# Kernel tuning notes

Measured on AMD Instinct MI355X. Metric: run time of the kernel, lower is better.

## Reference

```python
import jax, jax.numpy as jnp
import numpy as np


def setup_inputs() -> dict:
    key = jax.random.key(0)
    ks = jax.random.split(key, 4)
    B, C, D, H, W = 2, 128, 16, 16, 16
    scale = 1.0 / np.sqrt(C)
    x = jax.random.normal(ks[0], (B, C, D, H, W), dtype=jnp.float32)
    Wq = jax.random.normal(ks[1], (C, C), dtype=jnp.float32) * scale
    Wk = jax.random.normal(ks[2], (C, C), dtype=jnp.float32) * scale
    Wv = jax.random.normal(ks[3], (C, C), dtype=jnp.float32) * scale
    bq = jnp.zeros((C,), jnp.float32)
    bk = jnp.zeros((C,), jnp.float32)
    bv = jnp.zeros((C,), jnp.float32)
    gamma = jnp.asarray(0.3, jnp.float32)
    return {"x": x, "Wq": Wq, "bq": bq, "Wk": Wk, "bk": bk, "Wv": Wv, "bv": bv, "gamma": gamma}


def reference(x, Wq, bq, Wk, bk, Wv, bv, gamma):
    B, C, D, H, W = x.shape
    N = D * H * W
    xf = x.reshape(B, C, N)  # flatten spatial dims
    # 1x1x1 Conv3d == per-voxel channel mixing
    q = jnp.einsum('oc,bcn->bon', Wq, xf) + bq[:, None]
    k = jnp.einsum('oc,bcn->bon', Wk, xf) + bk[:, None]
    v = jnp.einsum('oc,bcn->bon', Wv, xf) + bv[:, None]
    # attn[b,n,m] = sum_c q[b,c,n] * k[b,c,m], custom 1.3 scale, softmax over m
    attn = jax.nn.softmax(jnp.einsum('bcn,bcm->bnm', q, k) * 1.3, axis=2)
    # out = v @ attn^T : out[b,c,n] = sum_m v[b,c,m] * attn[b,n,m]
    out = jnp.einsum('bcm,bnm->bcn', v, attn)
    return x + gamma * out.reshape(B, C, D, H, W)
```

## Files before the change

### kernel.cpp

```cpp
#include <hip/hip_runtime.h>
#include <hip/hip_bf16.h>

typedef __bf16 bf16x8 __attribute__((ext_vector_type(8)));
typedef __bf16 bf16x4 __attribute__((ext_vector_type(4)));
typedef float  floatx4 __attribute__((ext_vector_type(4)));


#define QSCALE 1.8755035f

__global__ __launch_bounds__(128) void proj_kernel(
    const float* __restrict__ x,
    const float* __restrict__ Wq, const float* __restrict__ bq,
    const float* __restrict__ Wk, const float* __restrict__ bk,
    const float* __restrict__ Wv, const float* __restrict__ bv,
    __bf16* __restrict__ qT, __bf16* __restrict__ kT, __bf16* __restrict__ vT2)
{
    constexpr int C = 128, N = 4096;
    const int b = blockIdx.z, which = blockIdx.y, n0 = blockIdx.x * 32;
    const int tid = threadIdx.x;
    const int wv = tid >> 6, lane = tid & 63, l15 = lane & 15, quad = lane >> 4;
    const float* W    = (which == 0) ? Wq : (which == 1) ? Wk : Wv;
    const float* bias = (which == 0) ? bq : (which == 1) ? bk : bv;

    __shared__ __bf16 xhi[32][136];
    __shared__ __bf16 xlo[32][136];
    __shared__ __bf16 v_lds[128][40];

    #pragma unroll
    for (int rep = 0; rep < 8; ++rep) {
        const int j = tid + rep * 128;
        const int c = j >> 3, nl4 = (j & 7) * 4;
        const float4 xv = *(const float4*)(x + (size_t)(b * C + c) * N + n0 + nl4);
        #pragma unroll
        for (int r = 0; r < 4; ++r) {
            const float v = (&xv.x)[r];
            const __bf16 h = (__bf16)v;
            xhi[nl4 + r][c] = h;
            xlo[nl4 + r][c] = (__bf16)(v - (float)h);
        }
    }
    __syncthreads();

    bf16x8 xbh[4], xbl[4];
    #pragma unroll
    for (int kk = 0; kk < 4; ++kk) {
        xbh[kk] = *(bf16x8*)(&xhi[wv * 16 + l15][kk * 32 + quad * 8]);
        xbl[kk] = *(bf16x8*)(&xlo[wv * 16 + l15][kk * 32 + quad * 8]);
    }

    floatx4 acc[8];
    const floatx4 fz = {0.f, 0.f, 0.f, 0.f};
    #pragma unroll
    for (int t = 0; t < 8; ++t) acc[t] = fz;

    #pragma unroll
    for (int kk = 0; kk < 4; ++kk)
        #pragma unroll
        for (int ct = 0; ct < 8; ++ct) {
            const float* wp = W + (size_t)(ct * 16 + l15) * C + kk * 32 + quad * 8;
            const float4 w0 = *(const float4*)wp;
            const float4 w1 = *(const float4*)(wp + 4);
            bf16x8 ahi, alo;
            #pragma unroll
            for (int r = 0; r < 4; ++r) {
                const float v0 = (&w0.x)[r]; const __bf16 h0 = (__bf16)v0;
                ahi[r] = h0; alo[r] = (__bf16)(v0 - (float)h0);
                const float v1 = (&w1.x)[r]; const __bf16 h1 = (__bf16)v1;
                ahi[4 + r] = h1; alo[4 + r] = (__bf16)(v1 - (float)h1);
            }
            acc[ct] = __builtin_amdgcn_mfma_f32_16x16x32_bf16(ahi, xbh[kk], acc[ct], 0, 0, 0);
            acc[ct] = __builtin_amdgcn_mfma_f32_16x16x32_bf16(alo, xbh[kk], acc[ct], 0, 0, 0);
            acc[ct] = __builtin_amdgcn_mfma_f32_16x16x32_bf16(ahi, xbl[kk], acc[ct], 0, 0, 0);
        }

    const int n = n0 + wv * 16 + l15;
    if (which < 2) {
        __bf16* dst = (which == 0) ? qT : kT;
        #pragma unroll
        for (int ct = 0; ct < 8; ++ct) {
            const float4 b4 = *(const float4*)(bias + ct * 16 + quad * 4);
            bf16x4 o;
            #pragma unroll
            for (int r = 0; r < 4; ++r) o[r] = (__bf16)(acc[ct][r] + (&b4.x)[r]);
            *(bf16x4*)(dst + (size_t)(b * N + n) * C + ct * 16 + quad * 4) = o;
        }
    } else {
        #pragma unroll
        for (int ct = 0; ct < 8; ++ct) {
            const float4 b4 = *(const float4*)(bias + ct * 16 + quad * 4);
            #pragma unroll
            for (int r = 0; r < 4; ++r)
                v_lds[ct * 16 + quad * 4 + r][wv * 16 + l15] = (__bf16)(acc[ct][r] + (&b4.x)[r]);
        }
        __syncthreads();
        #pragma unroll
        for (int rep = 0; rep < 4; ++rep) {
            const int j = tid + rep * 128;
            const int c = j >> 2, m8 = (j & 3) * 8;
            *(bf16x8*)(vT2 + (size_t)(b * C + c) * N + n0 + m8) = *(bf16x8*)(&v_lds[c][m8]);
        }
    }
}

template <int NSPLIT, bool PARTIAL>
__global__ __launch_bounds__(256, 2) void flash_kernel(
    const __bf16* __restrict__ qT, const __bf16* __restrict__ kT,
    const __bf16* __restrict__ vT2, const float* __restrict__ x,
    const float* __restrict__ gamma_p, __bf16* __restrict__ Opart,
    float* __restrict__ ml, float* __restrict__ out)
{
    constexpr int C = 128, N = 4096, Bn = 2;
    const int bid = blockIdx.x;
    const int r7 = bid & 7;
    const int b = r7 >> 2;
    const int rest = (bid >> 3) * 4 + (r7 & 3);
    const int nt = rest / NSPLIT, split = rest % NSPLIT;
    const int n0 = nt * 128;
    const int tid = threadIdx.x;
    const int wv = tid >> 6, lane = tid & 63, l15 = lane & 15, quad = lane >> 4;

    __shared__ __bf16 k_s[64][136];
    __shared__ __bf16 v_s[128][72];
    __shared__ __bf16 p_s[4][32][72];

    const int nA = n0 + wv * 32 + l15;
    bf16x8 qbA[4], qbB[4];
    #pragma unroll
    for (int kk = 0; kk < 4; ++kk) {
        qbA[kk] = *(const bf16x8*)(qT + (size_t)(b * N + nA) * C + kk * 32 + quad * 8);
        qbB[kk] = *(const bf16x8*)(qT + (size_t)(b * N + nA + 16) * C + kk * 32 + quad * 8);
    }

    float mA = -3.0e38f, lA = 0.f, mB = -3.0e38f, lB = 0.f;
    floatx4 OA[8], OB[8];
    const floatx4 fz = {0.f, 0.f, 0.f, 0.f};
    #pragma unroll
    for (int t = 0; t < 8; ++t) { OA[t] = fz; OB[t] = fz; }

    const __bf16* kB = kT  + (size_t)b * N * C;
    const __bf16* vB = vT2 + (size_t)b * C * N;
    constexpr int ITERS = (N / NSPLIT) / 64;
    const int mbeg = split * (N / NSPLIT);

    bf16x8 kpre[4], vpre[4];
    #pragma unroll
    for (int rep = 0; rep < 4; ++rep) {
        const int kj = tid + rep * 256;
        kpre[rep] = *(const bf16x8*)(kB + (size_t)(mbeg + (kj >> 4)) * C + (kj & 15) * 8);
        const int vj = tid + rep * 256;
        vpre[rep] = *(const bf16x8*)(vB + (size_t)(vj >> 3) * N + mbeg + (vj & 7) * 8);
    }

    for (int it = 0; it < ITERS; ++it) {
        __syncthreads();
        #pragma unroll
        for (int rep = 0; rep < 4; ++rep) {
            const int kj = tid + rep * 256;
            *(bf16x8*)(&k_s[kj >> 4][(kj & 15) * 8]) = kpre[rep];
            const int vj = tid + rep * 256;
            *(bf16x8*)(&v_s[vj >> 3][(vj & 7) * 8]) = vpre[rep];
        }
        __syncthreads();

        if (it + 1 < ITERS) {
            const int m1 = mbeg + (it + 1) * 64;
            #pragma unroll
            for (int rep = 0; rep < 4; ++rep) {
                const int kj = tid + rep * 256;
                kpre[rep] = *(const bf16x8*)(kB + (size_t)(m1 + (kj >> 4)) * C + (kj & 15) * 8);
                const int vj = tid + rep * 256;
                vpre[rep] = *(const bf16x8*)(vB + (size_t)(vj >> 3) * N + m1 + (vj & 7) * 8);
            }
        }

        floatx4 SA[4], SB[4];
        #pragma unroll
        for (int ct = 0; ct < 4; ++ct) { SA[ct] = fz; SB[ct] = fz; }
        #pragma unroll
        for (int kk = 0; kk < 4; ++kk)
            #pragma unroll
            for (int ct = 0; ct < 4; ++ct) {
                const bf16x8 a = *(bf16x8*)(&k_s[ct * 16 + l15][kk * 32 + quad * 8]);
                SA[ct] = __builtin_amdgcn_mfma_f32_16x16x32_bf16(a, qbA[kk], SA[ct], 0, 0, 0);
                SB[ct] = __builtin_amdgcn_mfma_f32_16x16x32_bf16(a, qbB[kk], SB[ct], 0, 0, 0);
            }

        float rmaxA = -3.0e38f, rmaxB = -3.0e38f;
        #pragma unroll
        for (int ct = 0; ct < 4; ++ct)
            #pragma unroll
            for (int r = 0; r < 4; ++r) {
                const float vA = SA[ct][r] * QSCALE; SA[ct][r] = vA; rmaxA = fmaxf(rmaxA, vA);
                const float vB2 = SB[ct][r] * QSCALE; SB[ct][r] = vB2; rmaxB = fmaxf(rmaxB, vB2);
            }
        rmaxA = fmaxf(rmaxA, __shfl_xor(rmaxA, 16, 64));
        rmaxA = fmaxf(rmaxA, __shfl_xor(rmaxA, 32, 64));
        rmaxB = fmaxf(rmaxB, __shfl_xor(rmaxB, 16, 64));
        rmaxB = fmaxf(rmaxB, __shfl_xor(rmaxB, 32, 64));

        const float mnA = fmaxf(mA, rmaxA);
        const float alphaA = exp2f(mA - mnA);
        mA = mnA;
        const float mnB = fmaxf(mB, rmaxB);
        const float alphaB = exp2f(mB - mnB);
        mB = mnB;

        float rsumA = 0.f, rsumB = 0.f;
        #pragma unroll
        for (int ct = 0; ct < 4; ++ct)
            #pragma unroll
            for (int r = 0; r < 4; ++r) {
                const float pA = exp2f(SA[ct][r] - mA); SA[ct][r] = pA; rsumA += pA;
                const float pB = exp2f(SB[ct][r] - mB); SB[ct][r] = pB; rsumB += pB;
            }
        rsumA += __shfl_xor(rsumA, 16, 64);
        rsumA += __shfl_xor(rsumA, 32, 64);
        rsumB += __shfl_xor(rsumB, 16, 64);
        rsumB += __shfl_xor(rsumB, 32, 64);
        lA = lA * alphaA + rsumA;
        lB = lB * alphaB + rsumB;

        #pragma unroll
        for (int t = 0; t < 8; ++t)
            #pragma unroll
            for (int r = 0; r < 4; ++r) { OA[t][r] *= alphaA; OB[t][r] *= alphaB; }

        #pragma unroll
        for (int ct = 0; ct < 4; ++ct) {
            bf16x4 pkA, pkB;
            #pragma unroll
            for (int r = 0; r < 4; ++r) { pkA[r] = (__bf16)SA[ct][r]; pkB[r] = (__bf16)SB[ct][r]; }
            *(bf16x4*)(&p_s[wv][l15][ct * 16 + quad * 4])      = pkA;
            *(bf16x4*)(&p_s[wv][16 + l15][ct * 16 + quad * 4]) = pkB;
        }

        #pragma unroll
        for (int kk = 0; kk < 2; ++kk) {
            const bf16x8 pbA = *(bf16x8*)(&p_s[wv][l15][kk * 32 + quad * 8]);
            const bf16x8 pbB = *(bf16x8*)(&p_s[wv][16 + l15][kk * 32 + quad * 8]);
            #pragma unroll
            for (int ct = 0; ct < 8; ++ct) {
                const bf16x8 a = *(bf16x8*)(&v_s[ct * 16 + l15][kk * 32 + quad * 8]);
                OA[ct] = __builtin_amdgcn_mfma_f32_16x16x32_bf16(a, pbA, OA[ct], 0, 0, 0);
                OB[ct] = __builtin_amdgcn_mfma_f32_16x16x32_bf16(a, pbB, OB[ct], 0, 0, 0);
            }
        }
    }

    if (PARTIAL) {
        __bf16* OpA = Opart + (((size_t)split * Bn + b) * N + nA) * C;
        __bf16* OpB = OpA + (size_t)16 * C;
        #pragma unroll
        for (int ct = 0; ct < 8; ++ct) {
            bf16x4 oA, oB;
            #pragma unroll
            for (int r = 0; r < 4; ++r) { oA[r] = (__bf16)OA[ct][r]; oB[r] = (__bf16)OB[ct][r]; }
            *(bf16x4*)(OpA + ct * 16 + quad * 4) = oA;
            *(bf16x4*)(OpB + ct * 16 + quad * 4) = oB;
        }
        if (quad == 0) {
            float* mlp = ml + (((size_t)split * Bn + b) * N + nA) * 2;
            mlp[0] = mA; mlp[1] = lA;
            mlp[32] = mB; mlp[33] = lB;
        }
    } else {
        const float scA = 1.f / lA, scB = 1.f / lB;
        const float gamma = gamma_p[0];
        #pragma unroll
        for (int ct = 0; ct < 8; ++ct)
            #pragma unroll
            for (int r = 0; r < 4; ++r) {
                const int c = ct * 16 + quad * 4 + r;
                const size_t iA = ((size_t)b * C + c) * N + nA;
                out[iA]      = x[iA]      + gamma * OA[ct][r] * scA;
                out[iA + 16] = x[iA + 16] + gamma * OB[ct][r] * scB;
            }
    }
}

template <int S>
__global__ __launch_bounds__(256) void combine_kernel(
    const __bf16* __restrict__ Opart, const float* __restrict__ ml,
    const float* __restrict__ x, const float* __restrict__ gamma_p,
    float* __restrict__ out)
{
    constexpr int C = 128, N = 4096, Bn = 2;
    const int b = blockIdx.y, n0 = blockIdx.x * 32;
    const int tid = threadIdx.x;
    __shared__ float cf[S][32];
    __shared__ float ot[32][132];

    if (tid < 32) {
        const int n = n0 + tid;
        float ms[S], ls[S];
        #pragma unroll
        for (int s = 0; s < S; ++s) {
            const float* mlp = ml + (((size_t)s * Bn + b) * N + n) * 2;
            ms[s] = mlp[0]; ls[s] = mlp[1];
        }
        float M = -3.0e38f;
        #pragma unroll
        for (int s = 0; s < S; ++s) M = fmaxf(M, ms[s]);
        float L = 0.f, e[S];
        #pragma unroll
        for (int s = 0; s < S; ++s) { e[s] = exp2f(ms[s] - M); L += e[s] * ls[s]; }
        const float inv = 1.f / L;
        #pragma unroll
        for (int s = 0; s < S; ++s) cf[s][tid] = e[s] * inv;
    }
    __syncthreads();

    #pragma unroll
    for (int rep = 0; rep < 2; ++rep) {
        const int j = tid + rep * 256;
        const int nl = j >> 4, c8 = (j & 15) * 8;
        float acc[8] = {0, 0, 0, 0, 0, 0, 0, 0};
        #pragma unroll
        for (int s = 0; s < S; ++s) {
            const float c0 = cf[s][nl];
            const bf16x8 ov = *(const bf16x8*)(Opart + (((size_t)s * Bn + b) * N + n0 + nl) * C + c8);
            #pragma unroll
            for (int t = 0; t < 8; ++t) acc[t] += c0 * (float)ov[t];
        }
        *(float4*)(&ot[nl][c8])     = *(float4*)(&acc[0]);
        *(float4*)(&ot[nl][c8 + 4]) = *(float4*)(&acc[4]);
    }
    __syncthreads();

    const int nl = tid & 31, cbase = tid >> 5;
    const float gamma = gamma_p[0];
    #pragma unroll
    for (int k = 0; k < 16; ++k) {
        const int c = cbase * 16 + k;
        const size_t idx = ((size_t)b * C + c) * N + n0 + nl;
        out[idx] = x[idx] + gamma * ot[nl][c];
    }
}

extern "C" void kernel_launch(void* const* d_in, const int* in_sizes, int n_in,
                              void* d_out, int out_size, void* d_ws, size_t ws_size,
                              hipStream_t stream) {
    const float* x     = (const float*)d_in[0];
    const float* Wq    = (const float*)d_in[1];
    const float* bq    = (const float*)d_in[2];
    const float* Wk    = (const float*)d_in[3];
    const float* bk    = (const float*)d_in[4];
    const float* Wv    = (const float*)d_in[5];
    const float* bv    = (const float*)d_in[6];
    const float* gamma = (const float*)d_in[7];
    float* out = (float*)d_out;

    constexpr int Bn = 2, C = 128, N = 4096;
    constexpr size_t QKV = (size_t)Bn * N * C;
    __bf16* qT    = (__bf16*)d_ws;
    __bf16* kT    = qT + QKV;
    __bf16* vT2   = kT + QKV;
    __bf16* Opart = vT2 + QKV;
    float* ml8 = (float*)(Opart + (size_t)8 * Bn * N * C);
    float* ml4 = (float*)(Opart + (size_t)4 * Bn * N * C);
    const size_t need8 = (char*)(ml8 + (size_t)8 * Bn * N * 2) - (char*)d_ws;
    const size_t need4 = (char*)(ml4 + (size_t)4 * Bn * N * 2) - (char*)d_ws;

    proj_kernel<<<dim3(N / 32, 3, Bn), 128, 0, stream>>>(
        x, Wq, bq, Wk, bk, Wv, bv, qT, kT, vT2);

    if (ws_size >= need8) {
        flash_kernel<8, true><<<32 * 8 * Bn, 256, 0, stream>>>(
            qT, kT, vT2, x, gamma, Opart, ml8, out);
        combine_kernel<8><<<dim3(N / 32, Bn), 256, 0, stream>>>(
            Opart, ml8, x, gamma, out);
    } else if (ws_size >= need4) {
        flash_kernel<4, true><<<32 * 4 * Bn, 256, 0, stream>>>(
            qT, kT, vT2, x, gamma, Opart, ml4, out);
        combine_kernel<4><<<dim3(N / 32, Bn), 256, 0, stream>>>(
            Opart, ml4, x, gamma, out);
    } else {
        flash_kernel<1, false><<<32 * 1 * Bn, 256, 0, stream>>>(
            qT, kT, vT2, x, gamma, nullptr, nullptr, out);
    }
}
```

Before: 125.7 us.

## Fuse split-K combine into flash kernel via last-block atomic counter

Removes the separate combine kernel launch. Each flash block now bumps an atomic per-tile counter, and the last split to finish merges all partial outputs and writes the final result. The QSCALE multiply is also moved off the max path and folded into the exp argument and alpha. This saves one kernel launch and its dependency gap, at the cost of a memset, fences, extra shared memory (which may reduce occupancy), and a serial tail in which a single block combines 128 rows.

```diff
diff --git a/kernel.cpp b/kernel.cpp
--- a/kernel.cpp
+++ b/kernel.cpp
@@ -107,7 +107,7 @@
     const __bf16* __restrict__ qT, const __bf16* __restrict__ kT,
     const __bf16* __restrict__ vT2, const float* __restrict__ x,
     const float* __restrict__ gamma_p, __bf16* __restrict__ Opart,
-    float* __restrict__ ml, float* __restrict__ out)
+    float* __restrict__ ml, int* __restrict__ cnt, float* __restrict__ out)
 {
     constexpr int C = 128, N = 4096, Bn = 2;
     const int bid = blockIdx.x;
@@ -122,6 +122,9 @@
     __shared__ __bf16 k_s[64][136];
     __shared__ __bf16 v_s[128][72];
     __shared__ __bf16 p_s[4][32][72];
+    __shared__ float cf[PARTIAL ? NSPLIT : 1][32];
+    __shared__ float ot[32][132];
+    __shared__ int s_old;
 
     const int nA = n0 + wv * 32 + l15;
     bf16x8 qbA[4], qbB[4];
@@ -190,8 +193,8 @@
         for (int ct = 0; ct < 4; ++ct)
             #pragma unroll
             for (int r = 0; r < 4; ++r) {
-                const float vA = SA[ct][r] * QSCALE; SA[ct][r] = vA; rmaxA = fmaxf(rmaxA, vA);
-                const float vB2 = SB[ct][r] * QSCALE; SB[ct][r] = vB2; rmaxB = fmaxf(rmaxB, vB2);
+                rmaxA = fmaxf(rmaxA, SA[ct][r]);
+                rmaxB = fmaxf(rmaxB, SB[ct][r]);
             }
         rmaxA = fmaxf(rmaxA, __shfl_xor(rmaxA, 16, 64));
         rmaxA = fmaxf(rmaxA, __shfl_xor(rmaxA, 32, 64));
@@ -199,19 +202,20 @@
         rmaxB = fmaxf(rmaxB, __shfl_xor(rmaxB, 32, 64));
 
         const float mnA = fmaxf(mA, rmaxA);
-        const float alphaA = exp2f(mA - mnA);
+        const float alphaA = exp2f((mA - mnA) * QSCALE);
         mA = mnA;
         const float mnB = fmaxf(mB, rmaxB);
-        const float alphaB = exp2f(mB - mnB);
+        const float alphaB = exp2f((mB - mnB) * QSCALE);
         mB = mnB;
+        const float qmA = mA * QSCALE, qmB = mB * QSCALE;
 
         float rsumA = 0.f, rsumB = 0.f;
         #pragma unroll
         for (int ct = 0; ct < 4; ++ct)
             #pragma unroll
             for (int r = 0; r < 4; ++r) {
-                const float pA = exp2f(SA[ct][r] - mA); SA[ct][r] = pA; rsumA += pA;
-                const float pB = exp2f(SB[ct][r] - mB); SB[ct][r] = pB; rsumB += pB;
+                const float pA = exp2f(SA[ct][r] * QSCALE - qmA); SA[ct][r] = pA; rsumA += pA;
+                const float pB = exp2f(SB[ct][r] * QSCALE - qmB); SB[ct][r] = pB; rsumB += pB;
             }
         rsumA += __shfl_xor(rsumA, 16, 64);
         rsumA += __shfl_xor(rsumA, 32, 64);
@@ -247,23 +251,7 @@
         }
     }
 
-    if (PARTIAL) {
-        __bf16* OpA = Opart + (((size_t)split * Bn + b) * N + nA) * C;
-        __bf16* OpB = OpA + (size_t)16 * C;
-        #pragma unroll
-        for (int ct = 0; ct < 8; ++ct) {
-            bf16x4 oA, oB;
-            #pragma unroll
-            for (int r = 0; r < 4; ++r) { oA[r] = (__bf16)OA[ct][r]; oB[r] = (__bf16)OB[ct][r]; }
-            *(bf16x4*)(OpA + ct * 16 + quad * 4) = oA;
-            *(bf16x4*)(OpB + ct * 16 + quad * 4) = oB;
-        }
-        if (quad == 0) {
-            float* mlp = ml + (((size_t)split * Bn + b) * N + nA) * 2;
-            mlp[0] = mA; mlp[1] = lA;
-            mlp[32] = mB; mlp[33] = lB;
-        }
-    } else {
+    if (!PARTIAL) {
         const float scA = 1.f / lA, scB = 1.f / lB;
         const float gamma = gamma_p[0];
         #pragma unroll
@@ -275,65 +263,82 @@
                 out[iA]      = x[iA]      + gamma * OA[ct][r] * scA;
                 out[iA + 16] = x[iA + 16] + gamma * OB[ct][r] * scB;
             }
-    }
-}
-
-template <int S>
-__global__ __launch_bounds__(256) void combine_kernel(
-    const __bf16* __restrict__ Opart, const float* __restrict__ ml,
-    const float* __restrict__ x, const float* __restrict__ gamma_p,
-    float* __restrict__ out)
-{
-    constexpr int C = 128, N = 4096, Bn = 2;
-    const int b = blockIdx.y, n0 = blockIdx.x * 32;
-    const int tid = threadIdx.x;
-    __shared__ float cf[S][32];
-    __shared__ float ot[32][132];
-
-    if (tid < 32) {
-        const int n = n0 + tid;
-        float ms[S], ls[S];
-        #pragma unroll
-        for (int s = 0; s < S; ++s) {
-            const float* mlp = ml + (((size_t)s * Bn + b) * N + n) * 2;
-            ms[s] = mlp[0]; ls[s] = mlp[1];
-        }
-        float M = -3.0e38f;
-        #pragma unroll
-        for (int s = 0; s < S; ++s) M = fmaxf(M, ms[s]);
-        float L = 0.f, e[S];
-        #pragma unroll
-        for (int s = 0; s < S; ++s) { e[s] = exp2f(ms[s] - M); L += e[s] * ls[s]; }
-        const float inv = 1.f / L;
-        #pragma unroll
-        for (int s = 0; s < S; ++s) cf[s][tid] = e[s] * inv;
-    }
+        return;
+    }
+
+    __bf16* OpA = Opart + (((size_t)split * Bn + b) * N + nA) * C;
+    __bf16* OpB = OpA + (size_t)16 * C;
+    #pragma unroll
+    for (int ct = 0; ct < 8; ++ct) {
+        bf16x4 oA, oB;
+        #pragma unroll
+        for (int r = 0; r < 4; ++r) { oA[r] = (__bf16)OA[ct][r]; oB[r] = (__bf16)OB[ct][r]; }
+        *(bf16x4*)(OpA + ct * 16 + quad * 4) = oA;
+        *(bf16x4*)(OpB + ct * 16 + quad * 4) = oB;
+    }
+    if (quad == 0) {
+        float* mlp = ml + (((size_t)split * Bn + b) * N + nA) * 2;
+        mlp[0] = mA; mlp[1] = lA;
+        mlp[32] = mB; mlp[33] = lB;
+    }
+
+    __threadfence();
+    if (tid == 0) s_old = atomicAdd(&cnt[b * 32 + nt], 1);
     __syncthreads();
-
-    #pragma unroll
-    for (int rep = 0; rep < 2; ++rep) {
-        const int j = tid + rep * 256;
-        const int nl = j >> 4, c8 = (j & 15) * 8;
-        float acc[8] = {0, 0, 0, 0, 0, 0, 0, 0};
-        #pragma unroll
-        for (int s = 0; s < S; ++s) {
-            const float c0 = cf[s][nl];
-            const bf16x8 ov = *(const bf16x8*)(Opart + (((size_t)s * Bn + b) * N + n0 + nl) * C + c8);
-            #pragma unroll
-            for (int t = 0; t < 8; ++t) acc[t] += c0 * (float)ov[t];
-        }
-        *(float4*)(&ot[nl][c8])     = *(float4*)(&acc[0]);
-        *(float4*)(&ot[nl][c8 + 4]) = *(float4*)(&acc[4]);
-    }
-    __syncthreads();
-
-    const int nl = tid & 31, cbase = tid >> 5;
+    if (s_old != NSPLIT - 1) return;
+    __threadfence();
+
     const float gamma = gamma_p[0];
-    #pragma unroll
-    for (int k = 0; k < 16; ++k) {
-        const int c = cbase * 16 + k;
-        const size_t idx = ((size_t)b * C + c) * N + n0 + nl;
-        out[idx] = x[idx] + gamma * ot[nl][c];
+    for (int qtr = 0; qtr < 4; ++qtr) {
+        const int nq = n0 + qtr * 32;
+        if (tid < 32) {
+            const int nn = nq + tid;
+            float ms[NSPLIT], ls[NSPLIT];
+            #pragma unroll
+            for (int s = 0; s < NSPLIT; ++s) {
+                const float* mlp = ml + (((size_t)s * Bn + b) * N + nn) * 2;
+                ms[s] = mlp[0]; ls[s] = mlp[1];
+            }
+            float M = -3.0e38f;
+            #pragma unroll
+            for (int s = 0; s < NSPLIT; ++s) M = fmaxf(M, ms[s]);
+            float L = 0.f, e[NSPLIT];
+            #pragma unroll
+            for (int s = 0; s < NSPLIT; ++s) {
+                e[s] = exp2f((ms[s] - M) * QSCALE);
+                L += e[s] * ls[s];
+            }
+            const float inv = 1.f / L;
+            #pragma unroll
+            for (int s = 0; s < NSPLIT; ++s) cf[s][tid] = e[s] * inv;
+        }
+        __syncthreads();
+
+        #pragma unroll
+        for (int rep = 0; rep < 2; ++rep) {
+            const int j = tid + rep * 256;
+            const int nl = j >> 4, c8 = (j & 15) * 8;
+            float acc[8] = {0, 0, 0, 0, 0, 0, 0, 0};
+            #pragma unroll
+            for (int s = 0; s < NSPLIT; ++s) {
+                const float c0 = cf[s][nl];
+                const bf16x8 ov = *(const bf16x8*)(Opart + (((size_t)s * Bn + b) * N + nq + nl) * C + c8);
+                #pragma unroll
+                for (int t = 0; t < 8; ++t) acc[t] += c0 * (float)ov[t];
+            }
+            *(float4*)(&ot[nl][c8])     = *(float4*)(&acc[0]);
+            *(float4*)(&ot[nl][c8 + 4]) = *(float4*)(&acc[4]);
+        }
+        __syncthreads();
+
+        const int nl = tid & 31, cbase = tid >> 5;
+        #pragma unroll
+        for (int k = 0; k < 16; ++k) {
+            const int c = cbase * 16 + k;
+            const size_t idx = ((size_t)b * C + c) * N + nq + nl;
+            out[idx] = x[idx] + gamma * ot[nl][c];
+        }
+        __syncthreads();
     }
 }
 
@@ -357,25 +362,25 @@
     __bf16* vT2   = kT + QKV;
     __bf16* Opart = vT2 + QKV;
     float* ml8 = (float*)(Opart + (size_t)8 * Bn * N * C);
+    int*   cnt8 = (int*)(ml8 + (size_t)8 * Bn * N * 2);
     float* ml4 = (float*)(Opart + (size_t)4 * Bn * N * C);
-    const size_t need8 = (char*)(ml8 + (size_t)8 * Bn * N * 2) - (char*)d_ws;
-    const size_t need4 = (char*)(ml4 + (size_t)4 * Bn * N * 2) - (char*)d_ws;
+    int*   cnt4 = (int*)(ml4 + (size_t)4 * Bn * N * 2);
+    const size_t need8 = (char*)(cnt8 + 64) - (char*)d_ws;
+    const size_t need4 = (char*)(cnt4 + 64) - (char*)d_ws;
 
     proj_kernel<<<dim3(N / 32, 3, Bn), 128, 0, stream>>>(
         x, Wq, bq, Wk, bk, Wv, bv, qT, kT, vT2);
 
     if (ws_size >= need8) {
+        hipMemsetAsync(cnt8, 0, 64 * sizeof(int), stream);
         flash_kernel<8, true><<<32 * 8 * Bn, 256, 0, stream>>>(
-            qT, kT, vT2, x, gamma, Opart, ml8, out);
-        combine_kernel<8><<<dim3(N / 32, Bn), 256, 0, stream>>>(
-            Opart, ml8, x, gamma, out);
+            qT, kT, vT2, x, gamma, Opart, ml8, cnt8, out);
     } else if (ws_size >= need4) {
+        hipMemsetAsync(cnt4, 0, 64 * sizeof(int), stream);
         flash_kernel<4, true><<<32 * 4 * Bn, 256, 0, stream>>>(
-            qT, kT, vT2, x, gamma, Opart, ml4, out);
-        combine_kernel<4><<<dim3(N / 32, Bn), 256, 0, stream>>>(
-            Opart, ml4, x, gamma, out);
+            qT, kT, vT2, x, gamma, Opart, ml4, cnt4, out);
     } else {
         flash_kernel<1, false><<<32 * 1 * Bn, 256, 0, stream>>>(
-            qT, kT, vT2, x, gamma, nullptr, nullptr, out);
+            qT, kT, vT2, x, gamma, nullptr, nullptr, nullptr, out);
     }
 }
```

After: 208.7 us. +66.0%, slower.
